# Kernel optimization log

Measured on AMD Instinct MI355X. Metric: run time of the kernel, lower is better.

The kernel has to match this reference:

```python
import jax, jax.numpy as jnp
import numpy as np

N_FEAT = 512
N_HEAD = 8
D_K = N_FEAT // N_HEAD


def setup_inputs() -> dict:
    key = jax.random.key(0)
    ks = jax.random.split(key, 10)
    B, S = 2, 4096
    scale = 1.0 / np.sqrt(N_FEAT)
    inp = {
        "x": jax.random.normal(ks[0], (B, S, N_FEAT), dtype=jnp.float32),
        "mask": jnp.zeros((B, 1, 1, S), dtype=jnp.float32),
        "wq": jax.random.normal(ks[1], (N_FEAT, N_FEAT), dtype=jnp.float32) * scale,
        "bq": jnp.zeros((N_FEAT,), dtype=jnp.float32),
        "wk": jax.random.normal(ks[2], (N_FEAT, N_FEAT), dtype=jnp.float32) * scale,
        "bk": jnp.zeros((N_FEAT,), dtype=jnp.float32),
        "wv": jax.random.normal(ks[3], (N_FEAT, N_FEAT), dtype=jnp.float32) * scale,
        "bv": jnp.zeros((N_FEAT,), dtype=jnp.float32),
        "wo": jax.random.normal(ks[4], (N_FEAT, N_FEAT), dtype=jnp.float32) * scale,
        "bo": jnp.zeros((N_FEAT,), dtype=jnp.float32),
    }
    return inp


def reference(x, mask, wq, bq, wk, bk, wv, bv, wo, bo):
    B, S, _ = x.shape
    # QKV projections (weights stored [in, out] = W^T of torch Linear)
    def proj(w, b):
        y = x @ w + b                      # [B, S, n_feat]
        y = y.reshape(B, S, N_HEAD, D_K)
        return y.transpose(0, 2, 1, 3)     # [B, H, S, d_k]
    q = proj(wq, bq)
    k = proj(wk, bk)
    v = proj(wv, bv)
    scores = jnp.einsum("bhsd,bhtd->bhst", q, k) / jnp.sqrt(jnp.float32(D_K))
    scores = scores + mask                 # additive mask, broadcast [B,1,1,S]
    attn = jax.nn.softmax(scores, axis=-1) # [B, H, S, S]
    ctx = jnp.einsum("bhst,bhtd->bhsd", attn, v)
    ctx = ctx.transpose(0, 2, 1, 3).reshape(B, S, N_FEAT)
    return ctx @ wo + bo
```

## Files before the change

kernel.cpp:

```cpp
#include <hip/hip_runtime.h>
#include <hip/hip_bf16.h>
#include <math.h>

#define SLEN 4096
#define NF   512
#define LOG2E 1.44269504f

typedef short s8v  __attribute__((ext_vector_type(8)));
typedef short s4v  __attribute__((ext_vector_type(4)));
typedef float f4v  __attribute__((ext_vector_type(4)));
typedef float f16v __attribute__((ext_vector_type(16)));

static __device__ __forceinline__ short f2bf(float f) {
  union { float f; unsigned int u; } v; v.f = f;
  unsigned int u = v.u;
  unsigned int r = (u + 0x7FFFu + ((u >> 16) & 1u)) >> 16;
  return (short)r;
}

__global__ __launch_bounds__(256) void prep_all(
    const float* __restrict__ x, const float* __restrict__ bq,
    const float* __restrict__ mask,
    short* __restrict__ xb, float* __restrict__ bqs, float* __restrict__ maskl) {
  const int b = blockIdx.x, tid = threadIdx.x;
  if (b < 2048) {
    size_t i = ((size_t)b * 256 + tid) * 8;
    float4 a = *(const float4*)(x + i);
    float4 c = *(const float4*)(x + i + 4);
    s8v o;
    o[0] = f2bf(a.x); o[1] = f2bf(a.y); o[2] = f2bf(a.z); o[3] = f2bf(a.w);
    o[4] = f2bf(c.x); o[5] = f2bf(c.y); o[6] = f2bf(c.z); o[7] = f2bf(c.w);
    *(s8v*)(xb + i) = o;
  } else if (b == 2048) {
#pragma unroll
    for (int j = 0; j < 2; j++) {
      int i = tid + 256 * j;
      bqs[i] = bq[i] * (0.125f * LOG2E);
    }
  } else {
    int i4 = ((b - 2049) * 1024) + tid * 4;
    float4 m = *(const float4*)(mask + i4);
    m.x *= LOG2E; m.y *= LOG2E; m.z *= LOG2E; m.w *= LOG2E;
    *(float4*)(maskl + i4) = m;
  }
}

__global__ __launch_bounds__(256) void prep_w(
    const float* __restrict__ wq, const float* __restrict__ wk,
    const float* __restrict__ wv, const float* __restrict__ wo,
    short* __restrict__ wt) {
  const int bz = blockIdx.y;
  const float* W = (bz == 0) ? wq : (bz == 1) ? wk : (bz == 2) ? wv : wo;
  const float scale = (bz == 0) ? 0.125f * LOG2E : 1.0f;
  const int tk = blockIdx.x & 7, tn = blockIdx.x >> 3;
  __shared__ short T[64][68];
  const int tid = threadIdx.x;
#pragma unroll
  for (int p = 0; p < 4; p++) {
    int c = tid + 256 * p;
    int kk = c >> 4, c4 = c & 15;
    float4 v = *(const float4*)(W + (size_t)(tk * 64 + kk) * NF + tn * 64 + c4 * 4);
    T[kk][c4 * 4 + 0] = f2bf(v.x * scale);
    T[kk][c4 * 4 + 1] = f2bf(v.y * scale);
    T[kk][c4 * 4 + 2] = f2bf(v.z * scale);
    T[kk][c4 * 4 + 3] = f2bf(v.w * scale);
  }
  __syncthreads();
#pragma unroll
  for (int p = 0; p < 2; p++) {
    int c = tid + 256 * p;
    int nrow = c >> 3, ks = c & 7;
    s8v g;
#pragma unroll
    for (int j = 0; j < 8; j++) g[j] = T[ks * 8 + j][nrow];
    *(s8v*)(wt + (size_t)bz * NF * NF + (size_t)(tn * 64 + nrow) * NF + tk * 64 + ks * 8) = g;
  }
}

__global__ __launch_bounds__(256) void qkv_proj(
    const short* __restrict__ xb, const short* __restrict__ wt,
    const float* __restrict__ bqs, const float* __restrict__ bk,
    const float* __restrict__ bv,
    short* __restrict__ qo, short* __restrict__ ko, short* __restrict__ vo)
{
  const int z = blockIdx.z;
  const short* WT   = wt + (size_t)z * NF * NF;
  const float* bias = (z == 0) ? bqs : (z == 1) ? bk : bv;
  const int m0 = blockIdx.x * 128;
  const int n0 = blockIdx.y * 128;

  __shared__ short Al[128][32];
  __shared__ short Bl[128][32];

  const int tid = threadIdx.x;
  const int wave = tid >> 6, lane = tid & 63;
  const int lg = lane >> 4, lr = lane & 15;
  const int wm = wave >> 1, wn = wave & 1;
  const int rsl = (lg ^ (lr & 3)) * 8;

  f4v acc[4][4];
#pragma unroll
  for (int i = 0; i < 4; i++)
#pragma unroll
    for (int j = 0; j < 4; j++) acc[i][j] = (f4v){0.f, 0.f, 0.f, 0.f};

  for (int k0 = 0; k0 < NF; k0 += 32) {
    __syncthreads();
#pragma unroll
    for (int i = 0; i < 2; i++) {
      int c = tid + 256 * i;
      int row = c >> 2, sl = c & 3;
      int wsl = (sl ^ (row & 3)) * 8;
      *(s8v*)&Al[row][wsl] = *(const s8v*)(xb + (size_t)(m0 + row) * NF + k0 + sl * 8);
      *(s8v*)&Bl[row][wsl] = *(const s8v*)(WT + (size_t)(n0 + row) * NF + k0 + sl * 8);
    }
    __syncthreads();

    s8v af[4], bf[4];
#pragma unroll
    for (int f = 0; f < 4; f++) af[f] = *(const s8v*)&Al[wm * 64 + f * 16 + lr][rsl];
#pragma unroll
    for (int f = 0; f < 4; f++) bf[f] = *(const s8v*)&Bl[wn * 64 + f * 16 + lr][rsl];
#pragma unroll
    for (int i = 0; i < 4; i++)
#pragma unroll
      for (int j = 0; j < 4; j++)
        acc[i][j] = __builtin_amdgcn_mfma_f32_16x16x32_bf16(af[i], bf[j], acc[i][j], 0, 0, 0);
  }

#pragma unroll
  for (int i = 0; i < 4; i++) {
    int mbase = m0 + wm * 64 + i * 16 + lg * 4;
#pragma unroll
    for (int j = 0; j < 4; j++) {
      int n = n0 + wn * 64 + j * 16 + lr;
      float bval = bias[n];
      int h = n >> 6, d = n & 63;
      if (z == 2) {
        int b = mbase >> 12, s = mbase & 4095;
        s4v pk;
#pragma unroll
        for (int r = 0; r < 4; r++) pk[r] = f2bf(acc[i][j][r] + bval);
        *(s4v*)(vo + ((size_t)((b * 8 + h) * 64 + d)) * SLEN + s) = pk;
      } else {
        short* dst = (z == 0) ? qo : ko;
#pragma unroll
        for (int r = 0; r < 4; r++) {
          int m = mbase + r;
          int b = m >> 12, s = m & 4095;
          dst[((size_t)((b * 8 + h)) * SLEN + s) * 64 + d] = f2bf(acc[i][j][r] + bval);
        }
      }
    }
  }
}

template<int SPLIT>
__global__ __launch_bounds__(256) void attn(
    const short* __restrict__ q, const short* __restrict__ k,
    const short* __restrict__ vt, const float* __restrict__ maskl,
    short* __restrict__ ctx, float* __restrict__ poa, float* __restrict__ plc)
{
  const int KVLEN = SLEN / SPLIT;
  const int NT = KVLEN / 64;
  __shared__ short Kl[2][64][64];
  __shared__ short Vl[2][64][64];

  const int tid = threadIdx.x;
  const int wave = tid >> 6, lane = tid & 63;
  const int h = lane >> 5, ln = lane & 31;

  const int x = blockIdx.x;
  const int c8 = x & 7, idx = x >> 3;
  const int bhsp = c8 + 8 * (idx >> 5);
  const int qb = idx & 31;
  const int bh = bhsp & 15;
  const int sp = bhsp >> 4;
  const int bb = bh >> 3, hh = bh & 7;
  const int q0 = qb * 128 + wave * 32;

  const short* qp = q + ((size_t)bh * SLEN + q0 + ln) * 64 + h * 8;
  s8v qf[4];
#pragma unroll
  for (int d = 0; d < 4; d++) qf[d] = *(const s8v*)(qp + d * 16);

  s8v ones;
#pragma unroll
  for (int j = 0; j < 8; j++) ones[j] = (short)0x3F80;

  f16v oa[2], lacc;
#pragma unroll
  for (int i = 0; i < 16; i++) { oa[0][i] = 0.f; oa[1][i] = 0.f; lacc[i] = 0.f; }

  const short* kg = k + (size_t)bh * SLEN * 64 + (size_t)sp * KVLEN * 64;
  const short* vg = vt + (size_t)bh * 64 * SLEN + (size_t)sp * KVLEN;
  const float* mp = maskl + (size_t)bb * SLEN + (size_t)sp * KVLEN;

  const int srow = tid >> 3, ss = tid & 7;
  const int sws = (ss ^ (srow & 7)) * 8;

  s8v kr0 = *(const s8v*)(kg + (size_t)srow * 64 + ss * 8);
  s8v kr1 = *(const s8v*)(kg + (size_t)(srow + 32) * 64 + ss * 8);
  s8v vr0 = *(const s8v*)(vg + (size_t)srow * SLEN + ss * 8);
  s8v vr1 = *(const s8v*)(vg + (size_t)(srow + 32) * SLEN + ss * 8);
  *(s8v*)&Kl[0][srow][sws] = kr0;  *(s8v*)&Kl[0][srow + 32][sws] = kr1;
  *(s8v*)&Vl[0][srow][sws] = vr0;  *(s8v*)&Vl[0][srow + 32][sws] = vr1;

  for (int it = 0; it < NT; ++it) {
    const int cur = it & 1;
    const int t0 = it * 64;
    __syncthreads();

    if (it + 1 < NT) {
      kr0 = *(const s8v*)(kg + (size_t)(t0 + 64 + srow) * 64 + ss * 8);
      kr1 = *(const s8v*)(kg + (size_t)(t0 + 96 + srow) * 64 + ss * 8);
      vr0 = *(const s8v*)(vg + (size_t)srow * SLEN + t0 + 64 + ss * 8);
      vr1 = *(const s8v*)(vg + (size_t)(srow + 32) * SLEN + t0 + 64 + ss * 8);
    }

    f16v sa[2];
#pragma unroll
    for (int tt = 0; tt < 2; tt++) {
#pragma unroll
      for (int q4 = 0; q4 < 4; q4++) {
        float4 mv = *(const float4*)(mp + t0 + tt * 32 + q4 * 8 + h * 4);
        sa[tt][q4 * 4 + 0] = mv.x;
        sa[tt][q4 * 4 + 1] = mv.y;
        sa[tt][q4 * 4 + 2] = mv.z;
        sa[tt][q4 * 4 + 3] = mv.w;
      }
    }
    __builtin_amdgcn_s_setprio(1);
#pragma unroll
    for (int tt = 0; tt < 2; tt++) {
#pragma unroll
      for (int ds_ = 0; ds_ < 4; ds_++) {
        s8v kf = *(const s8v*)&Kl[cur][tt * 32 + ln][(((ds_ * 2 + h) ^ (ln & 7))) * 8];
        sa[tt] = __builtin_amdgcn_mfma_f32_32x32x16_bf16(kf, qf[ds_], sa[tt], 0, 0, 0);
      }
    }
    __builtin_amdgcn_s_setprio(0);

    unsigned int pku[2][4][2];
#pragma unroll
    for (int tt = 0; tt < 2; tt++)
#pragma unroll
      for (int q4 = 0; q4 < 4; q4++) {
        float p0, p1, p2, p3;
        asm("v_exp_f32 %0, %1" : "=v"(p0) : "v"(sa[tt][q4 * 4 + 0]));
        asm("v_exp_f32 %0, %1" : "=v"(p1) : "v"(sa[tt][q4 * 4 + 1]));
        asm("v_exp_f32 %0, %1" : "=v"(p2) : "v"(sa[tt][q4 * 4 + 2]));
        asm("v_exp_f32 %0, %1" : "=v"(p3) : "v"(sa[tt][q4 * 4 + 3]));
        unsigned int u0, u1;
        asm("v_cvt_pk_bf16_f32 %0, %1, %2" : "=v"(u0) : "v"(p0), "v"(p1));
        asm("v_cvt_pk_bf16_f32 %0, %1, %2" : "=v"(u1) : "v"(p2), "v"(p3));
        pku[tt][q4][0] = u0;
        pku[tt][q4][1] = u1;
      }

    __builtin_amdgcn_s_setprio(1);
#pragma unroll
    for (int ks = 0; ks < 4; ks++) {
      const int tt = ks >> 1, k1 = ks & 1;
      unsigned int s0 = h ? pku[tt][2 * k1][0] : pku[tt][2 * k1 + 1][0];
      unsigned int s1 = h ? pku[tt][2 * k1][1] : pku[tt][2 * k1 + 1][1];
      unsigned int r0 = (unsigned int)__shfl_xor((int)s0, 32);
      unsigned int r1 = (unsigned int)__shfl_xor((int)s1, 32);
      union { unsigned int u[4]; s8v v; } af;
      af.u[0] = h ? r0 : pku[tt][2 * k1][0];
      af.u[1] = h ? r1 : pku[tt][2 * k1][1];
      af.u[2] = h ? pku[tt][2 * k1 + 1][0] : r0;
      af.u[3] = h ? pku[tt][2 * k1 + 1][1] : r1;
      lacc = __builtin_amdgcn_mfma_f32_32x32x16_bf16(af.v, ones, lacc, 0, 0, 0);
#pragma unroll
      for (int dt = 0; dt < 2; dt++) {
        s8v vf = *(const s8v*)&Vl[cur][dt * 32 + ln][(((ks * 2 + h) ^ (ln & 7))) * 8];
        oa[dt] = __builtin_amdgcn_mfma_f32_32x32x16_bf16(af.v, vf, oa[dt], 0, 0, 0);
      }
    }
    __builtin_amdgcn_s_setprio(0);

    if (it + 1 < NT) {
      *(s8v*)&Kl[cur ^ 1][srow][sws] = kr0;  *(s8v*)&Kl[cur ^ 1][srow + 32][sws] = kr1;
      *(s8v*)&Vl[cur ^ 1][srow][sws] = vr0;  *(s8v*)&Vl[cur ^ 1][srow + 32][sws] = vr1;
    }
  }

  if constexpr (SPLIT == 1) {
#pragma unroll
    for (int q4 = 0; q4 < 4; q4++)
#pragma unroll
      for (int i = 0; i < 4; i++) {
        float inv = 1.0f / lacc[q4 * 4 + i];
        int qrow = q0 + i + q4 * 8 + 4 * h;
        size_t base = ((size_t)bb * SLEN + qrow) * NF + hh * 64;
        ctx[base + ln]      = f2bf(oa[0][q4 * 4 + i] * inv);
        ctx[base + 32 + ln] = f2bf(oa[1][q4 * 4 + i] * inv);
      }
  } else {
#pragma unroll
    for (int dt = 0; dt < 2; dt++) {
      size_t dbase = ((size_t)(sp * 16 + bh) * 64 + dt * 32 + ln) * SLEN;
#pragma unroll
      for (int q4 = 0; q4 < 4; q4++) {
        float4 v = {oa[dt][q4 * 4 + 0], oa[dt][q4 * 4 + 1],
                    oa[dt][q4 * 4 + 2], oa[dt][q4 * 4 + 3]};
        *(float4*)(poa + dbase + q0 + q4 * 8 + 4 * h) = v;
      }
    }
    if (ln == 0) {
      size_t lbase = (size_t)(sp * 16 + bh) * SLEN;
#pragma unroll
      for (int q4 = 0; q4 < 4; q4++) {
        float4 v = {lacc[q4 * 4 + 0], lacc[q4 * 4 + 1],
                    lacc[q4 * 4 + 2], lacc[q4 * 4 + 3]};
        *(float4*)(plc + lbase + q0 + q4 * 8 + 4 * h) = v;
      }
    }
  }
}

__global__ __launch_bounds__(256) void out_proj(
    const short* __restrict__ ctx, const short* __restrict__ wt,
    const float* __restrict__ bo, float* __restrict__ out)
{
  const short* WT = wt + (size_t)3 * NF * NF;
  const int m0 = blockIdx.x * 128;
  const int n0 = blockIdx.y * 128;
  __shared__ short Al[128][32];
  __shared__ short Bl[128][32];
  const int tid = threadIdx.x;
  const int wave = tid >> 6, lane = tid & 63;
  const int lg = lane >> 4, lr = lane & 15;
  const int wm = wave >> 1, wn = wave & 1;
  const int rsl = (lg ^ (lr & 3)) * 8;

  f4v acc[4][4];
#pragma unroll
  for (int i = 0; i < 4; i++)
#pragma unroll
    for (int j = 0; j < 4; j++) acc[i][j] = (f4v){0.f, 0.f, 0.f, 0.f};

  for (int k0 = 0; k0 < NF; k0 += 32) {
    __syncthreads();
#pragma unroll
    for (int i = 0; i < 2; i++) {
      int c = tid + 256 * i;
      int row = c >> 2, sl = c & 3;
      int wsl = (sl ^ (row & 3)) * 8;
      *(s8v*)&Al[row][wsl] = *(const s8v*)(ctx + (size_t)(m0 + row) * NF + k0 + sl * 8);
      *(s8v*)&Bl[row][wsl] = *(const s8v*)(WT + (size_t)(n0 + row) * NF + k0 + sl * 8);
    }
    __syncthreads();

    s8v af[4], bf[4];
#pragma unroll
    for (int f = 0; f < 4; f++) af[f] = *(const s8v*)&Al[wm * 64 + f * 16 + lr][rsl];
#pragma unroll
    for (int f = 0; f < 4; f++) bf[f] = *(const s8v*)&Bl[wn * 64 + f * 16 + lr][rsl];
#pragma unroll
    for (int i = 0; i < 4; i++)
#pragma unroll
      for (int j = 0; j < 4; j++)
        acc[i][j] = __builtin_amdgcn_mfma_f32_16x16x32_bf16(af[i], bf[j], acc[i][j], 0, 0, 0);
  }

#pragma unroll
  for (int i = 0; i < 4; i++) {
    int mbase = m0 + wm * 64 + i * 16 + lg * 4;
#pragma unroll
    for (int j = 0; j < 4; j++) {
      int n = n0 + wn * 64 + j * 16 + lr;
      float bval = bo[n];
#pragma unroll
      for (int r = 0; r < 4; r++)
        out[(size_t)(mbase + r) * NF + n] = acc[i][j][r] + bval;
    }
  }
}

extern "C" void kernel_launch(void* const* d_in, const int* in_sizes, int n_in,
                              void* d_out, int out_size, void* d_ws, size_t ws_size,
                              hipStream_t stream) {
  const float* x    = (const float*)d_in[0];
  const float* mask = (const float*)d_in[1];
  const float* wq   = (const float*)d_in[2];
  const float* bq   = (const float*)d_in[3];
  const float* wk   = (const float*)d_in[4];
  const float* bk   = (const float*)d_in[5];
  const float* wv   = (const float*)d_in[6];
  const float* bv   = (const float*)d_in[7];
  const float* wo   = (const float*)d_in[8];
  const float* bo   = (const float*)d_in[9];
  float* out = (float*)d_out;

  char* ws = (char*)d_ws;
  const size_t MB = 1024ull * 1024ull;
  short* xb    = (short*)(ws);
  short* q_ws  = (short*)(ws + 8 * MB);
  short* k_ws  = (short*)(ws + 16 * MB);
  short* v_ws  = (short*)(ws + 24 * MB);
  short* c_ws  = (short*)(ws + 32 * MB);
  short* wt    = (short*)(ws + 40 * MB);
  float* bqs   = (float*)(ws + 42 * MB);
  float* maskl = (float*)(ws + 43 * MB);
  float* poa   = (float*)(ws + 44 * MB);
  float* plc   = (float*)(ws + 76 * MB);

  prep_all<<<2057, 256, 0, stream>>>(x, bq, mask, xb, bqs, maskl);
  prep_w<<<dim3(64, 4), 256, 0, stream>>>(wq, wk, wv, wo, wt);
  qkv_proj<<<dim3(64, 4, 3), 256, 0, stream>>>(xb, wt, bqs, bk, bv, q_ws, k_ws, v_ws);
  attn<1><<<512, 256, 0, stream>>>(q_ws, k_ws, v_ws, maskl, c_ws, poa, plc);
  out_proj<<<dim3(64, 4), 256, 0, stream>>>(c_ws, wt, bo, out);
}
```

Before: 159.0 us.

## Double-buffer projection GEMM tiles with direct global-to-LDS loads

The QKV and output projection GEMMs now copy tiles from global memory straight into LDS with global_load_lds. Each LDS tile is double-buffered so the next K-slice is fetched while MFMAs run on the current one, leaving one barrier per iteration instead of two. The goal is to hide global load latency and cut the register round-trip and barrier cost. In exchange the XOR swizzle is dropped, which can bring back LDS bank conflicts on fragment reads. Correctness also depends on the async LDS writes being waited on before the barrier.

```diff
diff --git a/kernel.cpp b/kernel.cpp
--- a/kernel.cpp
+++ b/kernel.cpp
@@ -10,6 +10,8 @@
 typedef short s4v  __attribute__((ext_vector_type(4)));
 typedef float f4v  __attribute__((ext_vector_type(4)));
 typedef float f16v __attribute__((ext_vector_type(16)));
+typedef __attribute__((address_space(1))) const unsigned int gu32;
+typedef __attribute__((address_space(3))) unsigned int lu32;
 
 static __device__ __forceinline__ short f2bf(float f) {
   union { float f; unsigned int u; } v; v.f = f;
@@ -89,14 +91,16 @@
   const int m0 = blockIdx.x * 128;
   const int n0 = blockIdx.y * 128;
 
-  __shared__ short Al[128][32];
-  __shared__ short Bl[128][32];
+  __shared__ short Al[2][128][32];
+  __shared__ short Bl[2][128][32];
 
   const int tid = threadIdx.x;
   const int wave = tid >> 6, lane = tid & 63;
   const int lg = lane >> 4, lr = lane & 15;
   const int wm = wave >> 1, wn = wave & 1;
-  const int rsl = (lg ^ (lr & 3)) * 8;
+
+  const int grow = lane >> 2;
+  const int gsl  = lane & 3;
 
   f4v acc[4][4];
 #pragma unroll
@@ -104,23 +108,41 @@
 #pragma unroll
     for (int j = 0; j < 4; j++) acc[i][j] = (f4v){0.f, 0.f, 0.f, 0.f};
 
-  for (int k0 = 0; k0 < NF; k0 += 32) {
+#pragma unroll
+  for (int c = 0; c < 2; c++) {
+    int row = wave * 32 + c * 16 + grow;
+    __builtin_amdgcn_global_load_lds(
+        (gu32*)(xb + (size_t)(m0 + row) * NF + gsl * 8),
+        (lu32*)&Al[0][wave * 32 + c * 16][0], 16, 0, 0);
+    __builtin_amdgcn_global_load_lds(
+        (gu32*)(WT + (size_t)(n0 + row) * NF + gsl * 8),
+        (lu32*)&Bl[0][wave * 32 + c * 16][0], 16, 0, 0);
+  }
+
+#pragma unroll
+  for (int ki = 0; ki < 16; ki++) {
+    const int cur = ki & 1;
     __syncthreads();
-#pragma unroll
-    for (int i = 0; i < 2; i++) {
-      int c = tid + 256 * i;
-      int row = c >> 2, sl = c & 3;
-      int wsl = (sl ^ (row & 3)) * 8;
-      *(s8v*)&Al[row][wsl] = *(const s8v*)(xb + (size_t)(m0 + row) * NF + k0 + sl * 8);
-      *(s8v*)&Bl[row][wsl] = *(const s8v*)(WT + (size_t)(n0 + row) * NF + k0 + sl * 8);
-    }
-    __syncthreads();
+
+    if (ki + 1 < 16) {
+      const int kn = (ki + 1) * 32;
+#pragma unroll
+      for (int c = 0; c < 2; c++) {
+        int row = wave * 32 + c * 16 + grow;
+        __builtin_amdgcn_global_load_lds(
+            (gu32*)(xb + (size_t)(m0 + row) * NF + kn + gsl * 8),
+            (lu32*)&Al[cur ^ 1][wave * 32 + c * 16][0], 16, 0, 0);
+        __builtin_amdgcn_global_load_lds(
+            (gu32*)(WT + (size_t)(n0 + row) * NF + kn + gsl * 8),
+            (lu32*)&Bl[cur ^ 1][wave * 32 + c * 16][0], 16, 0, 0);
+      }
+    }
 
     s8v af[4], bf[4];
 #pragma unroll
-    for (int f = 0; f < 4; f++) af[f] = *(const s8v*)&Al[wm * 64 + f * 16 + lr][rsl];
-#pragma unroll
-    for (int f = 0; f < 4; f++) bf[f] = *(const s8v*)&Bl[wn * 64 + f * 16 + lr][rsl];
+    for (int f = 0; f < 4; f++) af[f] = *(const s8v*)&Al[cur][wm * 64 + f * 16 + lr][lg * 8];
+#pragma unroll
+    for (int f = 0; f < 4; f++) bf[f] = *(const s8v*)&Bl[cur][wn * 64 + f * 16 + lr][lg * 8];
 #pragma unroll
     for (int i = 0; i < 4; i++)
 #pragma unroll
@@ -327,13 +349,14 @@
   const short* WT = wt + (size_t)3 * NF * NF;
   const int m0 = blockIdx.x * 128;
   const int n0 = blockIdx.y * 128;
-  __shared__ short Al[128][32];
-  __shared__ short Bl[128][32];
+  __shared__ short Al[2][128][32];
+  __shared__ short Bl[2][128][32];
   const int tid = threadIdx.x;
   const int wave = tid >> 6, lane = tid & 63;
   const int lg = lane >> 4, lr = lane & 15;
   const int wm = wave >> 1, wn = wave & 1;
-  const int rsl = (lg ^ (lr & 3)) * 8;
+  const int grow = lane >> 2;
+  const int gsl  = lane & 3;
 
   f4v acc[4][4];
 #pragma unroll
@@ -341,23 +364,41 @@
 #pragma unroll
     for (int j = 0; j < 4; j++) acc[i][j] = (f4v){0.f, 0.f, 0.f, 0.f};
 
-  for (int k0 = 0; k0 < NF; k0 += 32) {
+#pragma unroll
+  for (int c = 0; c < 2; c++) {
+    int row = wave * 32 + c * 16 + grow;
+    __builtin_amdgcn_global_load_lds(
+        (gu32*)(ctx + (size_t)(m0 + row) * NF + gsl * 8),
+        (lu32*)&Al[0][wave * 32 + c * 16][0], 16, 0, 0);
+    __builtin_amdgcn_global_load_lds(
+        (gu32*)(WT + (size_t)(n0 + row) * NF + gsl * 8),
+        (lu32*)&Bl[0][wave * 32 + c * 16][0], 16, 0, 0);
+  }
+
+#pragma unroll
+  for (int ki = 0; ki < 16; ki++) {
+    const int cur = ki & 1;
     __syncthreads();
-#pragma unroll
-    for (int i = 0; i < 2; i++) {
-      int c = tid + 256 * i;
-      int row = c >> 2, sl = c & 3;
-      int wsl = (sl ^ (row & 3)) * 8;
-      *(s8v*)&Al[row][wsl] = *(const s8v*)(ctx + (size_t)(m0 + row) * NF + k0 + sl * 8);
-      *(s8v*)&Bl[row][wsl] = *(const s8v*)(WT + (size_t)(n0 + row) * NF + k0 + sl * 8);
-    }
-    __syncthreads();
+
+    if (ki + 1 < 16) {
+      const int kn = (ki + 1) * 32;
+#pragma unroll
+      for (int c = 0; c < 2; c++) {
+        int row = wave * 32 + c * 16 + grow;
+        __builtin_amdgcn_global_load_lds(
+            (gu32*)(ctx + (size_t)(m0 + row) * NF + kn + gsl * 8),
+            (lu32*)&Al[cur ^ 1][wave * 32 + c * 16][0], 16, 0, 0);
+        __builtin_amdgcn_global_load_lds(
+            (gu32*)(WT + (size_t)(n0 + row) * NF + kn + gsl * 8),
+            (lu32*)&Bl[cur ^ 1][wave * 32 + c * 16][0], 16, 0, 0);
+      }
+    }
 
     s8v af[4], bf[4];
 #pragma unroll
-    for (int f = 0; f < 4; f++) af[f] = *(const s8v*)&Al[wm * 64 + f * 16 + lr][rsl];
-#pragma unroll
-    for (int f = 0; f < 4; f++) bf[f] = *(const s8v*)&Bl[wn * 64 + f * 16 + lr][rsl];
+    for (int f = 0; f < 4; f++) af[f] = *(const s8v*)&Al[cur][wm * 64 + f * 16 + lr][lg * 8];
+#pragma unroll
+    for (int f = 0; f < 4; f++) bf[f] = *(const s8v*)&Bl[cur][wn * 64 + f * 16 + lr][lg * 8];
 #pragma unroll
     for (int i = 0; i < 4; i++)
 #pragma unroll
```

Result: faster. 148.6 us (-6.5%).
